# Optimization experiments

Hardware: AMD Instinct MI355X
Metric: run time of the kernel (lower is better)

## Reference

```python
import jax, jax.numpy as jnp
import numpy as np

NUM_SEGMENTS = 24  # static max number of sentence segments (matches segment_ids fill_max)


def setup_inputs() -> dict:
    key = jax.random.key(0)
    k1, k2, k3 = jax.random.split(key, 3)
    B, L, S, D = 32, 4, 512, 768
    embeddings = jax.random.normal(k1, (B, L, S, D), dtype=jnp.float32)
    # word index of each subword token (sorted, as produced by left-to-right '##' merging)
    token_group_ids = jnp.sort(jax.random.randint(k2, (B, S), 0, 300), axis=1).astype(jnp.int32)
    # sentence-segment id of each (aggregated) word position (sorted, from '.'-cumsum)
    segment_ids = jnp.sort(jax.random.randint(k3, (B, S), 0, NUM_SEGMENTS), axis=1).astype(jnp.int32)
    return {"embeddings": embeddings, "token_group_ids": token_group_ids, "segment_ids": segment_ids}


def _segsum(data, seg_ids, num_segments):
    # data: [S, D], seg_ids: [S] -> [num_segments, D]
    return jax.ops.segment_sum(data, seg_ids, num_segments=num_segments)


def reference(embeddings, token_group_ids, segment_ids):
    B, L, S, D = embeddings.shape
    # --- aggregate_tokens: scatter-sum subword embeddings into word slots, padded to S ---
    # vmap over batch and layer; word capacity = S (original pads agg_embs back to num_words)
    per_layer = jax.vmap(_segsum, in_axes=(0, None, None))          # over L
    per_batch = jax.vmap(per_layer, in_axes=(0, 0, None))           # over B
    word_layer = per_batch(embeddings, token_group_ids, S)          # [B, L, S, D]
    # --- sentence embedding: mean over (padded) word axis, then sum over layers ---
    sent_embeddings = word_layer.mean(axis=2).sum(axis=1)           # [B, D]
    # --- word embedding: sum over layers (aggregate_method='sum') ---
    word_embeddings = word_layer.sum(axis=1)                        # [B, S, D]
    # --- aggregate_segments: scatter-sum word embeddings into sentence segments ---
    seg_embeddings = jax.vmap(_segsum, in_axes=(0, 0, None))(
        word_embeddings, segment_ids, NUM_SEGMENTS)                 # [B, G, D]
    seg_num = segment_ids.max(axis=1) + 1                           # [B]
    seg_mask = jnp.arange(NUM_SEGMENTS)[None, :] >= seg_num[:, None]  # True = padded segment
    return word_embeddings, sent_embeddings, seg_embeddings, seg_mask
```

## Files before the change

kernel.cpp:

```cpp
#include <hip/hip_runtime.h>

#define BB 32
#define LL 4
#define SS 512
#define DD 768
#define D4 (DD / 4)
#define GG 24

typedef float floatx4 __attribute__((ext_vector_type(4)));

#define WB_STRIDE (SS + 1)
#define SB_STRIDE (GG + 1)

__global__ __launch_bounds__(SS) void bounds_kernel(
    const int* __restrict__ tg, const int* __restrict__ sg,
    int* __restrict__ wb, int* __restrict__ sb)
{
    __shared__ int ltg[SS];
    __shared__ int lsg[SS];
    const int b = blockIdx.x;
    const int t = threadIdx.x;
    ltg[t] = tg[b * SS + t];
    lsg[t] = sg[b * SS + t];
    __syncthreads();

    {
        int v = t, lo = 0, hi = SS;
        while (lo < hi) { int m = (lo + hi) >> 1; if (ltg[m] < v) lo = m + 1; else hi = m; }
        wb[b * WB_STRIDE + t] = lo;
        if (t == 0) wb[b * WB_STRIDE + SS] = SS;
    }
    if (t <= GG) {
        int v = t, lo = 0, hi = SS;
        while (lo < hi) { int m = (lo + hi) >> 1; if (lsg[m] < v) lo = m + 1; else hi = m; }
        sb[b * SB_STRIDE + t] = lo;
    }
}

__global__ __launch_bounds__(D4) void word_agg_kernel(
    const floatx4* __restrict__ emb, const int* __restrict__ wb, floatx4* __restrict__ word)
{
    const int g = blockIdx.x;
    const int b = blockIdx.y;
    const int lo = wb[b * WB_STRIDE + g];
    const int hi = wb[b * WB_STRIDE + g + 1];
    const int d = threadIdx.x;

    floatx4 acc = (floatx4)(0.f);
    for (int s = lo; s < hi; ++s) {
#pragma unroll
        for (int l = 0; l < LL; ++l) {
            floatx4 v = __builtin_nontemporal_load(
                &emb[((size_t)((b * LL + l) * SS + s)) * D4 + d]);
            acc += v;
        }
    }
    word[((size_t)(b * SS + g)) * D4 + d] = acc;
}

__global__ __launch_bounds__(D4) void seg_agg_kernel(
    const floatx4* __restrict__ word, const int* __restrict__ sb, floatx4* __restrict__ seg)
{
    const int t = blockIdx.x;
    const int b = blockIdx.y;
    const int lo = sb[b * SB_STRIDE + t];
    const int hi = sb[b * SB_STRIDE + t + 1];
    const int d = threadIdx.x;

    floatx4 acc = (floatx4)(0.f);
    for (int g = lo; g < hi; ++g) {
        acc += word[((size_t)(b * SS + g)) * D4 + d];
    }
    seg[((size_t)(b * GG + t)) * D4 + d] = acc;
}

__global__ __launch_bounds__(D4) void sent_mask_kernel(
    const floatx4* __restrict__ seg, const int* __restrict__ sg,
    floatx4* __restrict__ sent, float* __restrict__ mask)
{
    const int b = blockIdx.x;
    const int d = threadIdx.x;

    floatx4 acc = (floatx4)(0.f);
#pragma unroll
    for (int t = 0; t < GG; ++t) {
        acc += seg[((size_t)(b * GG + t)) * D4 + d];
    }
    acc *= (1.0f / (float)SS);
    sent[(size_t)b * D4 + d] = acc;

    if (d < GG) {
        const int seg_num = sg[b * SS + (SS - 1)] + 1;
        mask[b * GG + d] = (d >= seg_num) ? 1.0f : 0.0f;
    }
}

extern "C" void kernel_launch(void* const* d_in, const int* in_sizes, int n_in,
                              void* d_out, int out_size, void* d_ws, size_t ws_size,
                              hipStream_t stream) {
    const float* emb = (const float*)d_in[0];
    const int*   tg  = (const int*)d_in[1];
    const int*   sg  = (const int*)d_in[2];

    float* out  = (float*)d_out;
    float* word = out;
    float* sent = word + (size_t)BB * SS * DD;
    float* seg  = sent + (size_t)BB * DD;
    float* mask = seg  + (size_t)BB * GG * DD;

    int* wb = (int*)d_ws;
    int* sb = wb + BB * WB_STRIDE;

    bounds_kernel<<<BB, SS, 0, stream>>>(tg, sg, wb, sb);
    word_agg_kernel<<<dim3(SS, BB), D4, 0, stream>>>((const floatx4*)emb, wb, (floatx4*)word);
    seg_agg_kernel<<<dim3(GG, BB), D4, 0, stream>>>((const floatx4*)word, sb, (floatx4*)seg);
    sent_mask_kernel<<<BB, D4, 0, stream>>>((const floatx4*)seg, sg, (floatx4*)sent, mask);
}
```

Measured before the change: 298.1 us.

## Fuse segment aggregation into word kernel via atomic adds

Drops the separate segment-sum kernel and its segment bounds search. Each word-aggregation block now handles eight words and atomically adds each nonempty word's sum into its segment row, which is zeroed beforehand by a memset. This avoids re-reading the word output from memory and saves a launch. The cost is contended float atomics on few segment rows, nondeterministic summation order, and fewer, longer-running blocks.

```diff
diff --git a/kernel.cpp b/kernel.cpp
--- a/kernel.cpp
+++ b/kernel.cpp
@@ -6,72 +6,63 @@
 #define DD 768
 #define D4 (DD / 4)
 #define GG 24
+#define WPB 8
+#define NCHUNK (SS / WPB)
 
 typedef float floatx4 __attribute__((ext_vector_type(4)));
 
 #define WB_STRIDE (SS + 1)
-#define SB_STRIDE (GG + 1)
 
 __global__ __launch_bounds__(SS) void bounds_kernel(
-    const int* __restrict__ tg, const int* __restrict__ sg,
-    int* __restrict__ wb, int* __restrict__ sb)
+    const int* __restrict__ tg, int* __restrict__ wb)
 {
     __shared__ int ltg[SS];
-    __shared__ int lsg[SS];
     const int b = blockIdx.x;
     const int t = threadIdx.x;
     ltg[t] = tg[b * SS + t];
-    lsg[t] = sg[b * SS + t];
     __syncthreads();
 
-    {
-        int v = t, lo = 0, hi = SS;
-        while (lo < hi) { int m = (lo + hi) >> 1; if (ltg[m] < v) lo = m + 1; else hi = m; }
-        wb[b * WB_STRIDE + t] = lo;
-        if (t == 0) wb[b * WB_STRIDE + SS] = SS;
-    }
-    if (t <= GG) {
-        int v = t, lo = 0, hi = SS;
-        while (lo < hi) { int m = (lo + hi) >> 1; if (lsg[m] < v) lo = m + 1; else hi = m; }
-        sb[b * SB_STRIDE + t] = lo;
-    }
+    int v = t, lo = 0, hi = SS;
+    while (lo < hi) { int m = (lo + hi) >> 1; if (ltg[m] < v) lo = m + 1; else hi = m; }
+    wb[b * WB_STRIDE + t] = lo;
+    if (t == 0) wb[b * WB_STRIDE + SS] = SS;
 }
 
 __global__ __launch_bounds__(D4) void word_agg_kernel(
-    const floatx4* __restrict__ emb, const int* __restrict__ wb, floatx4* __restrict__ word)
+    const floatx4* __restrict__ emb, const int* __restrict__ wb,
+    const int* __restrict__ sgids, floatx4* __restrict__ word,
+    float* __restrict__ seg)
 {
-    const int g = blockIdx.x;
+    const int c = blockIdx.x;
     const int b = blockIdx.y;
-    const int lo = wb[b * WB_STRIDE + g];
-    const int hi = wb[b * WB_STRIDE + g + 1];
+    const int w0 = c * WPB;
     const int d = threadIdx.x;
+    const int* wrow = wb + b * WB_STRIDE + w0;
 
-    floatx4 acc = (floatx4)(0.f);
-    for (int s = lo; s < hi; ++s) {
+    for (int wi = 0; wi < WPB; ++wi) {
+        const int w = w0 + wi;
+        const int lo = wrow[wi];
+        const int hi = wrow[wi + 1];
+
+        floatx4 acc = (floatx4)(0.f);
+        for (int s = lo; s < hi; ++s) {
 #pragma unroll
-        for (int l = 0; l < LL; ++l) {
-            floatx4 v = __builtin_nontemporal_load(
-                &emb[((size_t)((b * LL + l) * SS + s)) * D4 + d]);
-            acc += v;
+            for (int l = 0; l < LL; ++l) {
+                acc += __builtin_nontemporal_load(
+                    &emb[((size_t)((b * LL + l) * SS + s)) * D4 + d]);
+            }
+        }
+        __builtin_nontemporal_store(acc, &word[((size_t)(b * SS + w)) * D4 + d]);
+
+        if (hi > lo) {
+            const int t = sgids[b * SS + w];
+            float* sp = seg + ((size_t)(b * GG + t)) * DD + d * 4;
+            unsafeAtomicAdd(sp + 0, acc.x);
+            unsafeAtomicAdd(sp + 1, acc.y);
+            unsafeAtomicAdd(sp + 2, acc.z);
+            unsafeAtomicAdd(sp + 3, acc.w);
         }
     }
-    word[((size_t)(b * SS + g)) * D4 + d] = acc;
-}
-
-__global__ __launch_bounds__(D4) void seg_agg_kernel(
-    const floatx4* __restrict__ word, const int* __restrict__ sb, floatx4* __restrict__ seg)
-{
-    const int t = blockIdx.x;
-    const int b = blockIdx.y;
-    const int lo = sb[b * SB_STRIDE + t];
-    const int hi = sb[b * SB_STRIDE + t + 1];
-    const int d = threadIdx.x;
-
-    floatx4 acc = (floatx4)(0.f);
-    for (int g = lo; g < hi; ++g) {
-        acc += word[((size_t)(b * SS + g)) * D4 + d];
-    }
-    seg[((size_t)(b * GG + t)) * D4 + d] = acc;
 }
 
 __global__ __launch_bounds__(D4) void sent_mask_kernel(
@@ -109,10 +100,10 @@
     float* mask = seg  + (size_t)BB * GG * DD;
 
     int* wb = (int*)d_ws;
-    int* sb = wb + BB * WB_STRIDE;
 
-    bounds_kernel<<<BB, SS, 0, stream>>>(tg, sg, wb, sb);
-    word_agg_kernel<<<dim3(SS, BB), D4, 0, stream>>>((const floatx4*)emb, wb, (floatx4*)word);
-    seg_agg_kernel<<<dim3(GG, BB), D4, 0, stream>>>((const floatx4*)word, sb, (floatx4*)seg);
+    hipMemsetAsync(seg, 0, (size_t)BB * GG * DD * sizeof(float), stream);
+    bounds_kernel<<<BB, SS, 0, stream>>>(tg, wb);
+    word_agg_kernel<<<dim3(NCHUNK, BB), D4, 0, stream>>>(
+        (const floatx4*)emb, wb, sg, (floatx4*)word, seg);
     sent_mask_kernel<<<BB, D4, 0, stream>>>((const floatx4*)seg, sg, (floatx4*)sent, mask);
 }
```

Result: slower. 335.4 us (+12.5%).
